# Optimization experiments

Hardware: AMD Instinct MI355X
Metric: run time of the kernel (lower is better)

The kernel has to match this reference:

```python
import jax, jax.numpy as jnp
import numpy as np


def setup_inputs() -> dict:
    key = jax.random.key(0)
    kq, kk, kv = jax.random.split(key, 3)
    B, H, S, d = 2, 16, 2048, 64
    return {
        "query": jax.random.normal(kq, (B, H, S, d), dtype=jnp.float32),
        "keys": jax.random.normal(kk, (B, H, S, d), dtype=jnp.float32),
        "vals": jax.random.normal(kv, (B, H, S, d), dtype=jnp.float32),
    }


def reference(query, keys, vals):
    # SE (RBF-like) kernel attention, include_magnitude=True, p=2, dropout=0 (eval).
    d = query.shape[-1]
    scale = 2.0 * (d ** 0.5)
    q2 = jnp.sum(query * query, axis=-1)  # [B,H,Sq] = ||q||^2
    k2 = jnp.sum(keys * keys, axis=-1)    # [B,H,Sk] = ||k||^2
    qk = jnp.einsum("bhqd,bhkd->bhqk", query, keys)  # [B,H,Sq,Sk]
    # ||q-k||^2 = ||q||^2 - 2 q.k + ||k||^2 ; clamp for numerical safety
    sq_dist = jnp.maximum(q2[..., :, None] - 2.0 * qk + k2[..., None, :], 0.0)
    dist = jnp.sqrt(sq_dist)  # L2 norm (NOT squared), as in torch.norm(diff, p=2)
    # preattn = -||q-k|| / (2 sqrt(d)) + (||q||^2 + ||k||^2) / (2 sqrt(d))
    preattn = (-dist + q2[..., :, None] + k2[..., None, :]) / scale
    attn = jax.nn.softmax(preattn, axis=-1)  # [B,H,Sq,Sk]
    return jnp.einsum("bhqk,bhkd->bhqd", attn, vals)
```

## Files before the change

kernel.cpp:

```cpp
#include <hip/hip_runtime.h>
#include <hip/hip_bf16.h>
#include <math.h>


typedef __attribute__((ext_vector_type(8))) short bf16x8;
typedef __attribute__((ext_vector_type(4))) float f32x4;

#define SEQ    2048
#define DIM    64
#define NHEAD  32
#define QBLK   128
#define KVB    64
#define NKT    (SEQ / KVB)
#define TILE_B 8192
#define C2     0.0901684403f
#define THR2   11.5415603f

__device__ __forceinline__ float fast_exp2(float x) { return __builtin_amdgcn_exp2f(x); }
__device__ __forceinline__ float fast_sqrt(float x) { return __builtin_amdgcn_sqrtf(x); }

__device__ __forceinline__ unsigned int f2bf(float f) {
    __hip_bfloat16 h = __float2bfloat16(f);
    unsigned short u;
    __builtin_memcpy(&u, &h, 2);
    return (unsigned int)u;
}

__device__ __forceinline__ void gl_lds16(const void* g, void* l) {
    __builtin_amdgcn_global_load_lds(
        (const __attribute__((address_space(1))) unsigned int*)g,
        (__attribute__((address_space(3))) unsigned int*)l, 16, 0, 0);
}

__global__ __launch_bounds__(256, 4)
void prep_kv(const float* __restrict__ Kg, const float* __restrict__ Vg,
             char* __restrict__ Kp, char* __restrict__ Vp,
             float* __restrict__ k2g, float* __restrict__ k2cg) {
    __shared__ char Kimg[TILE_B];
    __shared__ char Vimg[TILE_B];

    const int tid  = threadIdx.x;
    const int kt   = blockIdx.x;
    const int head = blockIdx.y;
    const size_t hb = (size_t)head * (SEQ * DIM);

    {
        const int row = tid >> 2;
        const int sc4 = tid & 3;
        const float* kp = Kg + hb + (size_t)(kt * KVB + row) * DIM + sc4 * 16;
        f32x4 a = *(const f32x4*)kp;
        f32x4 b = *(const f32x4*)(kp + 4);
        f32x4 c = *(const f32x4*)(kp + 8);
        f32x4 d = *(const f32x4*)(kp + 12);
        float part = 0.f;
#pragma unroll
        for (int j = 0; j < 4; ++j)
            part += a[j]*a[j] + b[j]*b[j] + c[j]*c[j] + d[j]*d[j];
        part += __shfl_xor(part, 1);
        part += __shfl_xor(part, 2);
        if (sc4 == 0) {
            k2g[head * SEQ + kt * KVB + row]  = part;
            k2cg[head * SEQ + kt * KVB + row] = part * C2;
        }
        bf16x8 p0, p1;
#pragma unroll
        for (int j = 0; j < 4; ++j) {
            p0[j]     = (short)f2bf(a[j]);
            p0[4 + j] = (short)f2bf(b[j]);
            p1[j]     = (short)f2bf(c[j]);
            p1[4 + j] = (short)f2bf(d[j]);
        }
        const int sw = (row & 7) << 4;
        const int wa = row * 128 + sc4 * 32;
        *(bf16x8*)(Kimg + (wa ^ sw))        = p0;
        *(bf16x8*)(Kimg + ((wa + 16) ^ sw)) = p1;
    }
    {
        const int vpr = tid & 31;
        const int vd0 = (tid >> 5) * 8;
        const float* vp = Vg + hb + (size_t)(kt * KVB + 2 * vpr) * DIM + vd0;
        f32x4 a0 = *(const f32x4*)vp;
        f32x4 a1 = *(const f32x4*)(vp + 4);
        f32x4 b0 = *(const f32x4*)(vp + DIM);
        f32x4 b1 = *(const f32x4*)(vp + DIM + 4);
#pragma unroll
        for (int j = 0; j < 8; ++j) {
            const float lo = (j < 4) ? a0[j] : a1[j - 4];
            const float hi = (j < 4) ? b0[j] : b1[j - 4];
            const unsigned int pk = f2bf(lo) | (f2bf(hi) << 16);
            const int d  = vd0 + j;
            const int wa = d * 128 + vpr * 4;
            *(unsigned int*)(Vimg + (wa ^ ((d & 7) << 4))) = pk;
        }
    }
    __syncthreads();
    char* kdst = Kp + (size_t)(head * NKT + kt) * TILE_B;
    char* vdst = Vp + (size_t)(head * NKT + kt) * TILE_B;
#pragma unroll
    for (int s = 0; s < 2; ++s) {
        *(f32x4*)(kdst + s * 4096 + tid * 16) = *(const f32x4*)(Kimg + s * 4096 + tid * 16);
        *(f32x4*)(vdst + s * 4096 + tid * 16) = *(const f32x4*)(Vimg + s * 4096 + tid * 16);
    }
}

__global__ __launch_bounds__(512, 4)
void se_attn_main(const float* __restrict__ Qg, const char* __restrict__ Kp,
                  const char* __restrict__ Vp, const float* __restrict__ k2g,
                  const float* __restrict__ k2cg, float* __restrict__ Og) {
    __shared__ char Kbuf[2][TILE_B];
    __shared__ char Vbuf[2][TILE_B];
    __shared__ char Pl[8][2048];

    const int tid = threadIdx.x;
    const int w   = tid >> 6;
    const int l   = tid & 63;
    const int lq  = l & 15;
    const int g   = l >> 4;
    const int head = blockIdx.y;
    const size_t hb = (size_t)head * (SEQ * DIM);
    const int q = blockIdx.x * QBLK + w * 16 + lq;
    char* Pw = Pl[w];
    const int swq = (lq & 7) << 4;

    const char*  Kph  = Kp + (size_t)head * NKT * TILE_B;
    const char*  Vph  = Vp + (size_t)head * NKT * TILE_B;
    const float* k2h  = k2g  + head * SEQ;
    const float* k2ch = k2cg + head * SEQ;

    bf16x8 qf[2];
    float q2 = 0.f;
#pragma unroll
    for (int h = 0; h < 2; ++h) {
        const float* qp = Qg + hb + (size_t)q * DIM + h * 32 + g * 8;
        f32x4 a = *(const f32x4*)qp;
        f32x4 b = *(const f32x4*)(qp + 4);
#pragma unroll
        for (int j = 0; j < 4; ++j) {
            q2 += a[j] * a[j] + b[j] * b[j];
            qf[h][j]     = (short)f2bf(a[j]);
            qf[h][4 + j] = (short)f2bf(b[j]);
        }
    }
    q2 += __shfl_xor(q2, 16);
    q2 += __shfl_xor(q2, 32);

    f32x4 ofr[4];
#pragma unroll
    for (int i = 0; i < 4; ++i) ofr[i] = (f32x4){0.f, 0.f, 0.f, 0.f};
    float m = -INFINITY, lsA = 0.f, lsB = 0.f;

    gl_lds16(Kph + tid * 16, Kbuf[0] + w * 1024);
    gl_lds16(Vph + tid * 16, Vbuf[0] + w * 1024);
    __syncthreads();

    int cur = 0;
    for (int kt = 0; kt < NKT; ++kt) {
        f32x4 k2v[4], kcv[4];
#pragma unroll
        for (int f = 0; f < 4; ++f) {
            k2v[f] = *(const f32x4*)(k2h  + kt * KVB + f * 16 + g * 4);
            kcv[f] = *(const f32x4*)(k2ch + kt * KVB + f * 16 + g * 4);
        }

        if (kt + 1 < NKT) {
            const char* ktp = Kph + (size_t)(kt + 1) * TILE_B;
            const char* vtp = Vph + (size_t)(kt + 1) * TILE_B;
            gl_lds16(ktp + tid * 16, Kbuf[cur ^ 1] + w * 1024);
            gl_lds16(vtp + tid * 16, Vbuf[cur ^ 1] + w * 1024);
        }

        const char* Kl = Kbuf[cur];
        const char* Vt = Vbuf[cur];

        f32x4 st[4];
#pragma unroll
        for (int f = 0; f < 4; ++f) st[f] = (f32x4){0.f, 0.f, 0.f, 0.f};
        __builtin_amdgcn_s_setprio(1);
#pragma unroll
        for (int f = 0; f < 4; ++f) {
#pragma unroll
            for (int h = 0; h < 2; ++h) {
                const int ra = (f * 16 + lq) * 128 + h * 64 + g * 16;
                bf16x8 kf = *(const bf16x8*)(Kl + (ra ^ swq));
                st[f] = __builtin_amdgcn_mfma_f32_16x16x32_bf16(kf, qf[h], st[f], 0, 0, 0);
            }
        }
        __builtin_amdgcn_s_setprio(0);

        float sc[4][4];
        float tmf[4];
#pragma unroll
        for (int f = 0; f < 4; ++f) {
#pragma unroll
            for (int r = 0; r < 4; ++r) {
                const float sq = fmaxf(fmaf(-2.f, st[f][r], q2 + k2v[f][r]), 0.f);
                sc[f][r] = fmaf(-C2, fast_sqrt(sq), kcv[f][r]);
            }
            tmf[f] = fmaxf(fmaxf(sc[f][0], sc[f][1]), fmaxf(sc[f][2], sc[f][3]));
        }
        float tmax = fmaxf(fmaxf(tmf[0], tmf[1]), fmaxf(tmf[2], tmf[3]));
        tmax = fmaxf(tmax, __shfl_xor(tmax, 16));
        tmax = fmaxf(tmax, __shfl_xor(tmax, 32));
        if (tmax > m + THR2) {
            const float scale = fast_exp2(m - tmax);
            m = tmax;
            lsA *= scale; lsB *= scale;
#pragma unroll
            for (int i = 0; i < 4; ++i) {
                ofr[i][0] *= scale; ofr[i][1] *= scale;
                ofr[i][2] *= scale; ofr[i][3] *= scale;
            }
        }
#pragma unroll
        for (int f = 0; f < 4; ++f) {
#pragma unroll
            for (int e = 0; e < 2; ++e) {
                const float p0 = fast_exp2(sc[f][2 * e]     - m);
                const float p1 = fast_exp2(sc[f][2 * e + 1] - m);
                lsA += p0; lsB += p1;
                const unsigned int pk = f2bf(p0) | (f2bf(p1) << 16);
                const int pr = 8 * f + 2 * g + e;
                const int wa = lq * 128 + pr * 4;
                *(unsigned int*)(Pw + (wa ^ swq)) = pk;
            }
        }

        bf16x8 pf[2];
#pragma unroll
        for (int h = 0; h < 2; ++h) {
            const int ra = lq * 128 + h * 64 + g * 16;
            pf[h] = *(const bf16x8*)(Pw + (ra ^ swq));
        }
        __builtin_amdgcn_s_setprio(1);
#pragma unroll
        for (int db = 0; db < 4; ++db) {
#pragma unroll
            for (int h = 0; h < 2; ++h) {
                const int ra = (db * 16 + lq) * 128 + h * 64 + g * 16;
                bf16x8 vf = *(const bf16x8*)(Vt + (ra ^ swq));
                ofr[db] = __builtin_amdgcn_mfma_f32_16x16x32_bf16(vf, pf[h], ofr[db], 0, 0, 0);
            }
        }
        __builtin_amdgcn_s_setprio(0);

        __syncthreads();
        cur ^= 1;
    }

    float lsum = lsA + lsB;
    lsum += __shfl_xor(lsum, 16);
    lsum += __shfl_xor(lsum, 32);
    const float inv = 1.f / lsum;
    float* op = Og + hb + (size_t)q * DIM;
#pragma unroll
    for (int db = 0; db < 4; ++db) {
        f32x4 v;
#pragma unroll
        for (int r = 0; r < 4; ++r) v[r] = ofr[db][r] * inv;
        *(f32x4*)(op + db * 16 + g * 4) = v;
    }
}

__global__ __launch_bounds__(256, 4)
void se_attn_mfma(const float* __restrict__ Qg, const float* __restrict__ Kg,
                  const float* __restrict__ Vg, float* __restrict__ Og) {
    __shared__ char  Kl[KVB * 128];
    __shared__ char  Vt[DIM * 128];
    __shared__ char  Pl[4][16 * 128];
    __shared__ float k2s[KVB];

    const int tid = threadIdx.x;
    const int w   = tid >> 6;
    const int l   = tid & 63;
    const int lq  = l & 15;
    const int g   = l >> 4;
    const size_t hb = (size_t)blockIdx.y * (SEQ * DIM);
    const int q = blockIdx.x * 64 + w * 16 + lq;
    char* Pw = Pl[w];
    const int swq = (lq & 7) << 4;

    bf16x8 qf[2];
    float q2 = 0.f;
#pragma unroll
    for (int h = 0; h < 2; ++h) {
        const float* qp = Qg + hb + (size_t)q * DIM + h * 32 + g * 8;
        f32x4 a = *(const f32x4*)qp;
        f32x4 b = *(const f32x4*)(qp + 4);
#pragma unroll
        for (int j = 0; j < 4; ++j) {
            q2 += a[j] * a[j] + b[j] * b[j];
            qf[h][j]     = (short)f2bf(a[j]);
            qf[h][4 + j] = (short)f2bf(b[j]);
        }
    }
    q2 += __shfl_xor(q2, 16);
    q2 += __shfl_xor(q2, 32);

    f32x4 ofr[4];
#pragma unroll
    for (int i = 0; i < 4; ++i) ofr[i] = (f32x4){0.f, 0.f, 0.f, 0.f};
    float m = -INFINITY, lsum = 0.f;

    const int srow = tid >> 2;
    const int sc4  = tid & 3;
    const int vpr  = tid & 31;
    const int vd0  = (tid >> 5) * 8;

    for (int kt = 0; kt < NKT; ++kt) {
        __syncthreads();
        {
            const float* kp = Kg + hb + (size_t)(kt * KVB + srow) * DIM + sc4 * 16;
            f32x4 a = *(const f32x4*)kp;
            f32x4 b = *(const f32x4*)(kp + 4);
            f32x4 c = *(const f32x4*)(kp + 8);
            f32x4 d = *(const f32x4*)(kp + 12);
            float part = 0.f;
#pragma unroll
            for (int j = 0; j < 4; ++j)
                part += a[j]*a[j] + b[j]*b[j] + c[j]*c[j] + d[j]*d[j];
            part += __shfl_xor(part, 1);
            part += __shfl_xor(part, 2);
            if (sc4 == 0) k2s[srow] = part;
            bf16x8 p0, p1;
#pragma unroll
            for (int j = 0; j < 4; ++j) {
                p0[j]     = (short)f2bf(a[j]);
                p0[4 + j] = (short)f2bf(b[j]);
                p1[j]     = (short)f2bf(c[j]);
                p1[4 + j] = (short)f2bf(d[j]);
            }
            const int sw = (srow & 7) << 4;
            const int wa = srow * 128 + sc4 * 32;
            *(bf16x8*)(Kl + (wa ^ sw))        = p0;
            *(bf16x8*)(Kl + ((wa + 16) ^ sw)) = p1;
        }
        {
            const float* vp = Vg + hb + (size_t)(kt * KVB + 2 * vpr) * DIM + vd0;
            f32x4 a0 = *(const f32x4*)vp;
            f32x4 a1 = *(const f32x4*)(vp + 4);
            f32x4 b0 = *(const f32x4*)(vp + DIM);
            f32x4 b1 = *(const f32x4*)(vp + DIM + 4);
#pragma unroll
            for (int j = 0; j < 8; ++j) {
                const float lo = (j < 4) ? a0[j] : a1[j - 4];
                const float hi = (j < 4) ? b0[j] : b1[j - 4];
                const unsigned int pk = f2bf(lo) | (f2bf(hi) << 16);
                const int d = vd0 + j;
                const int wa = d * 128 + vpr * 4;
                *(unsigned int*)(Vt + (wa ^ ((d & 7) << 4))) = pk;
            }
        }
        __syncthreads();

        f32x4 st[4];
#pragma unroll
        for (int f = 0; f < 4; ++f) st[f] = (f32x4){0.f, 0.f, 0.f, 0.f};
#pragma unroll
        for (int f = 0; f < 4; ++f) {
#pragma unroll
            for (int h = 0; h < 2; ++h) {
                const int ra = (f * 16 + lq) * 128 + h * 64 + g * 16;
                bf16x8 kf = *(const bf16x8*)(Kl + (ra ^ swq));
                st[f] = __builtin_amdgcn_mfma_f32_16x16x32_bf16(kf, qf[h], st[f], 0, 0, 0);
            }
        }

        float sc[4][4];
        float tmax = -INFINITY;
#pragma unroll
        for (int f = 0; f < 4; ++f) {
            const f32x4 k2v = *(const f32x4*)(k2s + f * 16 + g * 4);
#pragma unroll
            for (int r = 0; r < 4; ++r) {
                const float kk = k2v[r];
                const float sq = fmaxf(fmaf(-2.f, st[f][r], q2 + kk), 0.f);
                const float s  = (kk - sqrtf(sq)) * 0.0625f;
                sc[f][r] = s;
                tmax = fmaxf(tmax, s);
            }
        }
        tmax = fmaxf(tmax, __shfl_xor(tmax, 16));
        tmax = fmaxf(tmax, __shfl_xor(tmax, 32));
        const float nm    = fmaxf(m, tmax);
        const float scale = __expf(m - nm);
        m = nm;
        lsum *= scale;
#pragma unroll
        for (int i = 0; i < 4; ++i) {
            ofr[i][0] *= scale; ofr[i][1] *= scale;
            ofr[i][2] *= scale; ofr[i][3] *= scale;
        }
#pragma unroll
        for (int f = 0; f < 4; ++f) {
#pragma unroll
            for (int e = 0; e < 2; ++e) {
                const float p0 = __expf(sc[f][2 * e]     - m);
                const float p1 = __expf(sc[f][2 * e + 1] - m);
                lsum += p0 + p1;
                const unsigned int pk = f2bf(p0) | (f2bf(p1) << 16);
                const int pr = 8 * f + 2 * g + e;
                const int wa = lq * 128 + pr * 4;
                *(unsigned int*)(Pw + (wa ^ swq)) = pk;
            }
        }

        bf16x8 pf[2];
#pragma unroll
        for (int h = 0; h < 2; ++h) {
            const int ra = lq * 128 + h * 64 + g * 16;
            pf[h] = *(const bf16x8*)(Pw + (ra ^ swq));
        }
#pragma unroll
        for (int db = 0; db < 4; ++db) {
#pragma unroll
            for (int h = 0; h < 2; ++h) {
                const int ra = (db * 16 + lq) * 128 + h * 64 + g * 16;
                bf16x8 vf = *(const bf16x8*)(Vt + (ra ^ swq));
                ofr[db] = __builtin_amdgcn_mfma_f32_16x16x32_bf16(vf, pf[h], ofr[db], 0, 0, 0);
            }
        }
    }

    lsum += __shfl_xor(lsum, 16);
    lsum += __shfl_xor(lsum, 32);
    const float inv = 1.f / lsum;
    float* op = Og + hb + (size_t)q * DIM;
#pragma unroll
    for (int db = 0; db < 4; ++db) {
#pragma unroll
        for (int r = 0; r < 4; ++r) {
            op[db * 16 + g * 4 + r] = ofr[db][r] * inv;
        }
    }
}

extern "C" void kernel_launch(void* const* d_in, const int* in_sizes, int n_in,
                              void* d_out, int out_size, void* d_ws, size_t ws_size,
                              hipStream_t stream) {
    const float* Q = (const float*)d_in[0];
    const float* K = (const float*)d_in[1];
    const float* V = (const float*)d_in[2];
    float* O = (float*)d_out;

    const size_t KP_B = (size_t)NHEAD * NKT * TILE_B;
    const size_t K2_B = (size_t)NHEAD * SEQ * 4;
    const size_t need = 2 * KP_B + 2 * K2_B;

    if (ws_size >= need) {
        char*  Kp  = (char*)d_ws;
        char*  Vp  = Kp + KP_B;
        float* k2  = (float*)(Kp + 2 * KP_B);
        float* k2c = (float*)((char*)k2 + K2_B);
        prep_kv<<<dim3(NKT, NHEAD), 256, 0, stream>>>(K, V, Kp, Vp, k2, k2c);
        se_attn_main<<<dim3(SEQ / QBLK, NHEAD), 512, 0, stream>>>(Q, Kp, Vp, k2, k2c, O);
    } else {
        se_attn_mfma<<<dim3(SEQ / 64, NHEAD), 256, 0, stream>>>(Q, K, V, O);
    }
}
```

Measured before the change: 97.93 us.

## Process two 16-row query tiles per wave to reuse K/V fragments

After: 100.8 us. 2.9% more time.

```diff
diff --git a/kernel.cpp b/kernel.cpp
--- a/kernel.cpp
+++ b/kernel.cpp
@@ -103,13 +103,13 @@
     }
 }
 
-__global__ __launch_bounds__(512, 4)
+__global__ __launch_bounds__(256, 2)
 void se_attn_main(const float* __restrict__ Qg, const char* __restrict__ Kp,
                   const char* __restrict__ Vp, const float* __restrict__ k2g,
                   const float* __restrict__ k2cg, float* __restrict__ Og) {
     __shared__ char Kbuf[2][TILE_B];
     __shared__ char Vbuf[2][TILE_B];
-    __shared__ char Pl[8][2048];
+    __shared__ char Pl[4][4096];
 
     const int tid = threadIdx.x;
     const int w   = tid >> 6;
@@ -118,7 +118,7 @@
     const int g   = l >> 4;
     const int head = blockIdx.y;
     const size_t hb = (size_t)head * (SEQ * DIM);
-    const int q = blockIdx.x * QBLK + w * 16 + lq;
+    const int qbase = blockIdx.x * QBLK + w * 32;
     char* Pw = Pl[w];
     const int swq = (lq & 7) << 4;
 
@@ -127,30 +127,40 @@
     const float* k2h  = k2g  + head * SEQ;
     const float* k2ch = k2cg + head * SEQ;
 
-    bf16x8 qf[2];
-    float q2 = 0.f;
-#pragma unroll
-    for (int h = 0; h < 2; ++h) {
-        const float* qp = Qg + hb + (size_t)q * DIM + h * 32 + g * 8;
-        f32x4 a = *(const f32x4*)qp;
-        f32x4 b = *(const f32x4*)(qp + 4);
-#pragma unroll
-        for (int j = 0; j < 4; ++j) {
-            q2 += a[j] * a[j] + b[j] * b[j];
-            qf[h][j]     = (short)f2bf(a[j]);
-            qf[h][4 + j] = (short)f2bf(b[j]);
-        }
-    }
-    q2 += __shfl_xor(q2, 16);
-    q2 += __shfl_xor(q2, 32);
-
-    f32x4 ofr[4];
-#pragma unroll
-    for (int i = 0; i < 4; ++i) ofr[i] = (f32x4){0.f, 0.f, 0.f, 0.f};
-    float m = -INFINITY, lsA = 0.f, lsB = 0.f;
-
-    gl_lds16(Kph + tid * 16, Kbuf[0] + w * 1024);
-    gl_lds16(Vph + tid * 16, Vbuf[0] + w * 1024);
+    bf16x8 qf[2][2];
+    float q2v[2];
+#pragma unroll
+    for (int j = 0; j < 2; ++j) {
+        float q2 = 0.f;
+#pragma unroll
+        for (int h = 0; h < 2; ++h) {
+            const float* qp = Qg + hb + (size_t)(qbase + j * 16 + lq) * DIM + h * 32 + g * 8;
+            f32x4 a = *(const f32x4*)qp;
+            f32x4 b = *(const f32x4*)(qp + 4);
+#pragma unroll
+            for (int e = 0; e < 4; ++e) {
+                q2 += a[e] * a[e] + b[e] * b[e];
+                qf[h][j][e]     = (short)f2bf(a[e]);
+                qf[h][j][4 + e] = (short)f2bf(b[e]);
+            }
+        }
+        q2 += __shfl_xor(q2, 16);
+        q2 += __shfl_xor(q2, 32);
+        q2v[j] = q2;
+    }
+
+    f32x4 ofr[4][2];
+#pragma unroll
+    for (int i = 0; i < 4; ++i)
+#pragma unroll
+        for (int j = 0; j < 2; ++j) ofr[i][j] = (f32x4){0.f, 0.f, 0.f, 0.f};
+    float m = -INFINITY, ls0 = 0.f, ls1 = 0.f;
+
+#pragma unroll
+    for (int s = 0; s < 2; ++s) {
+        gl_lds16(Kph + s * 4096 + tid * 16, Kbuf[0] + s * 4096 + w * 1024);
+        gl_lds16(Vph + s * 4096 + tid * 16, Vbuf[0] + s * 4096 + w * 1024);
+    }
     __syncthreads();
 
     int cur = 0;
@@ -165,16 +175,21 @@
         if (kt + 1 < NKT) {
             const char* ktp = Kph + (size_t)(kt + 1) * TILE_B;
             const char* vtp = Vph + (size_t)(kt + 1) * TILE_B;
-            gl_lds16(ktp + tid * 16, Kbuf[cur ^ 1] + w * 1024);
-            gl_lds16(vtp + tid * 16, Vbuf[cur ^ 1] + w * 1024);
+#pragma unroll
+            for (int s = 0; s < 2; ++s) {
+                gl_lds16(ktp + s * 4096 + tid * 16, Kbuf[cur ^ 1] + s * 4096 + w * 1024);
+                gl_lds16(vtp + s * 4096 + tid * 16, Vbuf[cur ^ 1] + s * 4096 + w * 1024);
+            }
         }
 
         const char* Kl = Kbuf[cur];
         const char* Vt = Vbuf[cur];
 
-        f32x4 st[4];
-#pragma unroll
-        for (int f = 0; f < 4; ++f) st[f] = (f32x4){0.f, 0.f, 0.f, 0.f};
+        f32x4 st[4][2];
+#pragma unroll
+        for (int f = 0; f < 4; ++f)
+#pragma unroll
+            for (int j = 0; j < 2; ++j) st[f][j] = (f32x4){0.f, 0.f, 0.f, 0.f};
         __builtin_amdgcn_s_setprio(1);
 #pragma unroll
         for (int f = 0; f < 4; ++f) {
@@ -182,21 +197,28 @@
             for (int h = 0; h < 2; ++h) {
                 const int ra = (f * 16 + lq) * 128 + h * 64 + g * 16;
                 bf16x8 kf = *(const bf16x8*)(Kl + (ra ^ swq));
-                st[f] = __builtin_amdgcn_mfma_f32_16x16x32_bf16(kf, qf[h], st[f], 0, 0, 0);
+                st[f][0] = __builtin_amdgcn_mfma_f32_16x16x32_bf16(kf, qf[h][0], st[f][0], 0, 0, 0);
+                st[f][1] = __builtin_amdgcn_mfma_f32_16x16x32_bf16(kf, qf[h][1], st[f][1], 0, 0, 0);
             }
         }
         __builtin_amdgcn_s_setprio(0);
 
-        float sc[4][4];
+        float sc[2][4][4];
         float tmf[4];
 #pragma unroll
         for (int f = 0; f < 4; ++f) {
-#pragma unroll
-            for (int r = 0; r < 4; ++r) {
-                const float sq = fmaxf(fmaf(-2.f, st[f][r], q2 + k2v[f][r]), 0.f);
-                sc[f][r] = fmaf(-C2, fast_sqrt(sq), kcv[f][r]);
-            }
-            tmf[f] = fmaxf(fmaxf(sc[f][0], sc[f][1]), fmaxf(sc[f][2], sc[f][3]));
+            float t0, t1;
+#pragma unroll
+            for (int j = 0; j < 2; ++j) {
+#pragma unroll
+                for (int r = 0; r < 4; ++r) {
+                    const float sq = fmaxf(fmaf(-2.f, st[f][j][r], q2v[j] + k2v[f][r]), 0.f);
+                    sc[j][f][r] = fmaf(-C2, fast_sqrt(sq), kcv[f][r]);
+                }
+            }
+            t0 = fmaxf(fmaxf(sc[0][f][0], sc[0][f][1]), fmaxf(sc[0][f][2], sc[0][f][3]));
+            t1 = fmaxf(fmaxf(sc[1][f][0], sc[1][f][1]), fmaxf(sc[1][f][2], sc[1][f][3]));
+            tmf[f] = fmaxf(t0, t1);
         }
         float tmax = fmaxf(fmaxf(tmf[0], tmf[1]), fmaxf(tmf[2], tmf[3]));
         tmax = fmaxf(tmax, __shfl_xor(tmax, 16));
@@ -204,33 +226,40 @@
         if (tmax > m + THR2) {
             const float scale = fast_exp2(m - tmax);
             m = tmax;
-            lsA *= scale; lsB *= scale;
-#pragma unroll
-            for (int i = 0; i < 4; ++i) {
-                ofr[i][0] *= scale; ofr[i][1] *= scale;
-                ofr[i][2] *= scale; ofr[i][3] *= scale;
-            }
-        }
-#pragma unroll
-        for (int f = 0; f < 4; ++f) {
-#pragma unroll
-            for (int e = 0; e < 2; ++e) {
-                const float p0 = fast_exp2(sc[f][2 * e]     - m);
-                const float p1 = fast_exp2(sc[f][2 * e + 1] - m);
-                lsA += p0; lsB += p1;
-                const unsigned int pk = f2bf(p0) | (f2bf(p1) << 16);
-                const int pr = 8 * f + 2 * g + e;
-                const int wa = lq * 128 + pr * 4;
-                *(unsigned int*)(Pw + (wa ^ swq)) = pk;
-            }
-        }
-
-        bf16x8 pf[2];
-#pragma unroll
-        for (int h = 0; h < 2; ++h) {
-            const int ra = lq * 128 + h * 64 + g * 16;
-            pf[h] = *(const bf16x8*)(Pw + (ra ^ swq));
-        }
+            ls0 *= scale; ls1 *= scale;
+#pragma unroll
+            for (int i = 0; i < 4; ++i)
+#pragma unroll
+                for (int j = 0; j < 2; ++j) {
+                    ofr[i][j][0] *= scale; ofr[i][j][1] *= scale;
+                    ofr[i][j][2] *= scale; ofr[i][j][3] *= scale;
+                }
+        }
+#pragma unroll
+        for (int j = 0; j < 2; ++j) {
+#pragma unroll
+            for (int f = 0; f < 4; ++f) {
+#pragma unroll
+                for (int e = 0; e < 2; ++e) {
+                    const float p0 = fast_exp2(sc[j][f][2 * e]     - m);
+                    const float p1 = fast_exp2(sc[j][f][2 * e + 1] - m);
+                    if (j == 0) ls0 += p0 + p1; else ls1 += p0 + p1;
+                    const unsigned int pk = f2bf(p0) | (f2bf(p1) << 16);
+                    const int pr = 8 * f + 2 * g + e;
+                    const int wa = (j * 16 + lq) * 128 + pr * 4;
+                    *(unsigned int*)(Pw + (wa ^ swq)) = pk;
+                }
+            }
+        }
+
+        bf16x8 pf[2][2];
+#pragma unroll
+        for (int j = 0; j < 2; ++j)
+#pragma unroll
+            for (int h = 0; h < 2; ++h) {
+                const int ra = (j * 16 + lq) * 128 + h * 64 + g * 16;
+                pf[j][h] = *(const bf16x8*)(Pw + (ra ^ swq));
+            }
         __builtin_amdgcn_s_setprio(1);
 #pragma unroll
         for (int db = 0; db < 4; ++db) {
@@ -238,7 +267,8 @@
             for (int h = 0; h < 2; ++h) {
                 const int ra = (db * 16 + lq) * 128 + h * 64 + g * 16;
                 bf16x8 vf = *(const bf16x8*)(Vt + (ra ^ swq));
-                ofr[db] = __builtin_amdgcn_mfma_f32_16x16x32_bf16(vf, pf[h], ofr[db], 0, 0, 0);
+                ofr[db][0] = __builtin_amdgcn_mfma_f32_16x16x32_bf16(vf, pf[0][h], ofr[db][0], 0, 0, 0);
+                ofr[db][1] = __builtin_amdgcn_mfma_f32_16x16x32_bf16(vf, pf[1][h], ofr[db][1], 0, 0, 0);
             }
         }
         __builtin_amdgcn_s_setprio(0);
@@ -247,17 +277,20 @@
         cur ^= 1;
     }
 
-    float lsum = lsA + lsB;
-    lsum += __shfl_xor(lsum, 16);
-    lsum += __shfl_xor(lsum, 32);
-    const float inv = 1.f / lsum;
-    float* op = Og + hb + (size_t)q * DIM;
-#pragma unroll
-    for (int db = 0; db < 4; ++db) {
-        f32x4 v;
-#pragma unroll
-        for (int r = 0; r < 4; ++r) v[r] = ofr[db][r] * inv;
-        *(f32x4*)(op + db * 16 + g * 4) = v;
+#pragma unroll
+    for (int j = 0; j < 2; ++j) {
+        float lsum = (j == 0) ? ls0 : ls1;
+        lsum += __shfl_xor(lsum, 16);
+        lsum += __shfl_xor(lsum, 32);
+        const float inv = 1.f / lsum;
+        float* op = Og + hb + (size_t)(qbase + j * 16 + lq) * DIM;
+#pragma unroll
+        for (int db = 0; db < 4; ++db) {
+            f32x4 v;
+#pragma unroll
+            for (int r = 0; r < 4; ++r) v[r] = ofr[db][j][r] * inv;
+            *(f32x4*)(op + db * 16 + g * 4) = v;
+        }
     }
 }
 
@@ -452,7 +485,7 @@
         float* k2  = (float*)(Kp + 2 * KP_B);
         float* k2c = (float*)((char*)k2 + K2_B);
         prep_kv<<<dim3(NKT, NHEAD), 256, 0, stream>>>(K, V, Kp, Vp, k2, k2c);
-        se_attn_main<<<dim3(SEQ / QBLK, NHEAD), 512, 0, stream>>>(Q, Kp, Vp, k2, k2c, O);
+        se_attn_main<<<dim3(SEQ / QBLK, NHEAD), 256, 0, stream>>>(Q, Kp, Vp, k2, k2c, O);
     } else {
         se_attn_mfma<<<dim3(SEQ / 64, NHEAD), 256, 0, stream>>>(Q, K, V, O);
     }
```
